# Kernel optimization log

Measured on AMD Instinct MI355X. Metric: run time of the kernel, lower is better.

The kernel has to match this reference:

```python
import jax, jax.numpy as jnp
import numpy as np

N_NODES = 100000
EPS = 1e-12  # F.normalize eps


def mean_aggregate(x, src, dst):
    # gather source features along edges, segment-mean into destinations
    msg = x[src]                                              # [E, D]
    summed = jax.ops.segment_sum(msg, dst, num_segments=N_NODES)  # [N, D]
    cnt = jax.ops.segment_sum(jnp.ones_like(dst, dtype=x.dtype), dst,
                              num_segments=N_NODES)           # [N]
    return summed / jnp.maximum(cnt, 1.0)[:, None]


def sage_conv(x, src, dst, W_l, b_l, W_r, normalize):
    agg = mean_aggregate(x, src, dst)
    out = agg @ W_l.T + b_l + x @ W_r.T  # lin_l(mean neigh) + lin_r(root)
    if normalize:
        norm = jnp.sqrt(jnp.sum(out * out, axis=-1, keepdims=True))
        out = out / jnp.maximum(norm, EPS)
    return out


def setup_inputs() -> dict:
    key = jax.random.key(0)
    ks = jax.random.split(key, 8)
    H, O = 128, 128
    s = 1.0 / np.sqrt(H)
    x = jax.random.normal(ks[0], (N_NODES, H), dtype=jnp.float32)
    edge_index = jax.random.randint(ks[1], (2, 1600000), 0, N_NODES, dtype=jnp.int64)
    return {
        "x": x,
        "edge_index": edge_index,
        "W1l": jax.random.uniform(ks[2], (H, H), jnp.float32, -s, s),
        "b1": jax.random.uniform(ks[3], (H,), jnp.float32, -s, s),
        "W1r": jax.random.uniform(ks[4], (H, H), jnp.float32, -s, s),
        "W2l": jax.random.uniform(ks[5], (O, H), jnp.float32, -s, s),
        "b2": jax.random.uniform(ks[6], (O,), jnp.float32, -s, s),
        "W2r": jax.random.uniform(ks[7], (O, H), jnp.float32, -s, s),
    }


def reference(x, edge_index, W1l, b1, W1r, W2l, b2, W2r):
    src, dst = edge_index[0], edge_index[1]
    h = sage_conv(x, src, dst, W1l, b1, W1r, normalize=True)
    h = jax.nn.relu(h)
    out = sage_conv(h, src, dst, W2l, b2, W2r, normalize=False)
    return out
```

## Files before the change

kernel.cpp:

```cpp
#include <hip/hip_runtime.h>
#include <hip/hip_bf16.h>
#include <hip/hip_fp16.h>

#define N_NODES 100000
#define DFEAT 128
#define SLAB 4096
#define BSHIFT 9
#define NBUCK 196

#define WS_CNT      0
#define WS_W16      100000
#define WS_BCNT     180000
#define WS_BBASE    180200
#define WS_BCUR     180400
#define WS_OFFS     200000
#define WS_ESRC     300608
#define WS_AGGH     1900608
#define WS_CASTH    8300608

typedef _Float16 half8 __attribute__((ext_vector_type(8)));
typedef _Float16 half2v __attribute__((ext_vector_type(2)));
typedef float floatx4 __attribute__((ext_vector_type(4)));

__global__ __launch_bounds__(256) void prep_kernel(const float* __restrict__ x,
                                                   __half* __restrict__ xh, int total4,
                                                   const int* __restrict__ dst,
                                                   int* __restrict__ bcnt,
                                                   const float* __restrict__ W1l,
                                                   const float* __restrict__ W1r,
                                                   const float* __restrict__ W2l,
                                                   const float* __restrict__ W2r,
                                                   __half* __restrict__ w16,
                                                   int E, int bpart, int castblocks) {
    __shared__ int lh[NBUCK];
    int b = blockIdx.x;
    if (b < castblocks) {
        int i = b * 256 + threadIdx.x;
        if (i < total4) {
            float4 v = ((const float4*)x)[i];
            __half2 h01 = __floats2half2_rn(v.x, v.y);
            __half2 h23 = __floats2half2_rn(v.z, v.w);
            uint2 o;
            o.x = *(unsigned int*)&h01;
            o.y = *(unsigned int*)&h23;
            ((uint2*)xh)[i] = o;
        }
        return;
    }
    if (b < castblocks + 64) {
        int i = (b - castblocks) * 256 + threadIdx.x;
        int m = i >> 12;
        int off = i & 4095;
        const float* Wp = (m == 0) ? W1l : (m == 1) ? W1r : (m == 2) ? W2l : W2r;
        float4 v = ((const float4*)Wp)[off];
        __half2 h01 = __floats2half2_rn(v.x, v.y);
        __half2 h23 = __floats2half2_rn(v.z, v.w);
        uint2 o;
        o.x = *(unsigned int*)&h01;
        o.y = *(unsigned int*)&h23;
        ((uint2*)w16)[i] = o;
        return;
    }
    int bb = b - castblocks - 64;
    for (int i = threadIdx.x; i < NBUCK; i += 256) lh[i] = 0;
    __syncthreads();
    int s0 = bb * SLAB, s1 = min(E, s0 + SLAB);
    for (int i = s0 + threadIdx.x; i < s1; i += 256)
        atomicAdd(&lh[dst[i] >> BSHIFT], 1);
    __syncthreads();
    for (int i = threadIdx.x; i < NBUCK; i += 256)
        if (lh[i] > 0) atomicAdd(&bcnt[i], lh[i]);
}

__global__ void bscan_kernel(const int* __restrict__ bcnt, int* __restrict__ bbase,
                             int* __restrict__ bcur, int E) {
    __shared__ int s[256];
    int t = threadIdx.x;
    int v = (t < NBUCK) ? bcnt[t] : 0;
    s[t] = v;
    __syncthreads();
    for (int d = 1; d < 256; d <<= 1) {
        int u = (t >= d) ? s[t - d] : 0;
        __syncthreads();
        s[t] += u;
        __syncthreads();
    }
    if (t < NBUCK) {
        int excl = s[t] - v;
        bbase[t] = excl;
        bcur[t] = excl;
    }
    if (t == 0) bbase[NBUCK] = E;
}

__global__ __launch_bounds__(256) void phase2_kernel(const int* __restrict__ src,
                                                     const int* __restrict__ dst,
                                                     int* __restrict__ bcur,
                                                     int2* __restrict__ pairs,
                                                     int E) {
    __shared__ int lbase[NBUCK];
    __shared__ int lcur[NBUCK];
    __shared__ int lgb[NBUCK];
    __shared__ int sc[256];
    __shared__ int2 lp[SLAB];
    int b = blockIdx.x;
    int t = threadIdx.x;
    for (int i = t; i < NBUCK; i += 256) lbase[i] = 0;
    __syncthreads();
    int s0 = b * SLAB, s1 = min(E, s0 + SLAB);
    for (int i = s0 + t; i < s1; i += 256)
        atomicAdd(&lbase[dst[i] >> BSHIFT], 1);
    __syncthreads();
    int v = (t < NBUCK) ? lbase[t] : 0;
    sc[t] = v;
    __syncthreads();
    for (int d = 1; d < 256; d <<= 1) {
        int u = (t >= d) ? sc[t - d] : 0;
        __syncthreads();
        sc[t] += u;
        __syncthreads();
    }
    if (t < NBUCK) {
        int excl = sc[t] - v;
        lbase[t] = excl;
        lcur[t] = excl;
        lgb[t] = (v > 0) ? atomicAdd(&bcur[t], v) : 0;
    }
    __syncthreads();
    for (int i = s0 + t; i < s1; i += 256) {
        int d = dst[i];
        int s = src[i];
        int bk = d >> BSHIFT;
        int pos = atomicAdd(&lcur[bk], 1);
        lp[pos] = make_int2(s, d);
    }
    __syncthreads();
    int m = s1 - s0;
    for (int i = t; i < m; i += 256) {
        int2 p = lp[i];
        int bk = p.y >> BSHIFT;
        pairs[lgb[bk] + (i - lbase[bk])] = p;
    }
}

__global__ __launch_bounds__(512) void phase3_kernel(const int2* __restrict__ pairs,
                                                     const int* __restrict__ bbase,
                                                     int* __restrict__ cnt,
                                                     int* __restrict__ offs,
                                                     int* __restrict__ esrc,
                                                     int n) {
    __shared__ int lcnt[512];
    __shared__ int sc[512];
    __shared__ int lexcl[512];
    int g = blockIdx.x;
    int node0 = g << BSHIFT;
    int t = threadIdx.x;
    lcnt[t] = 0;
    __syncthreads();
    int S = bbase[g];
    int Eg = bbase[g + 1];
    for (int i = S + t; i < Eg; i += 512)
        atomicAdd(&lcnt[pairs[i].y - node0], 1);
    __syncthreads();
    int v = lcnt[t];
    sc[t] = v;
    __syncthreads();
    for (int d = 1; d < 512; d <<= 1) {
        int u = (t >= d) ? sc[t - d] : 0;
        __syncthreads();
        sc[t] += u;
        __syncthreads();
    }
    int excl = sc[t] - v;
    lexcl[t] = excl;
    int nd = node0 + t;
    if (nd < n) {
        cnt[nd] = v;
        offs[nd] = S + excl;
    }
    __syncthreads();
    for (int i = S + t; i < Eg; i += 512) {
        int2 p = pairs[i];
        int pos = atomicAdd(&lexcl[p.y - node0], 1);
        esrc[S + pos] = p.x;
    }
}

#define ACC(c, r)                        \
    s[c][0] += *(half2v*)&(r).x;         \
    s[c][1] += *(half2v*)&(r).y;         \
    s[c][2] += *(half2v*)&(r).z;         \
    s[c][3] += *(half2v*)&(r).w;

__global__ void aggregate_kernel(const __half* __restrict__ feat, const int* __restrict__ esrc,
                                 const int* __restrict__ offs, const int* __restrict__ cnt,
                                 __half* __restrict__ agg, int n) {
    int wid = (blockIdx.x * blockDim.x + threadIdx.x) >> 6;
    int lane = threadIdx.x & 63;
    int grp = lane >> 4;
    int l15 = lane & 15;
    int node = wid * 4 + grp;
    if (node >= n) return;
    int beg = offs[node];
    int deg = cnt[node];
    const _Float16* fbase = (const _Float16*)feat + l15 * 8;
    const int* ep = esrc + beg;

    half2v s[4][4];
#pragma unroll
    for (int c = 0; c < 4; c++)
#pragma unroll
        for (int k = 0; k < 4; k++) s[c][k] = (half2v)(_Float16)0;

    int j = 0;
    for (; j + 8 <= deg; j += 8) {
        int i0 = ep[j + 0], i1 = ep[j + 1], i2 = ep[j + 2], i3 = ep[j + 3];
        int i4 = ep[j + 4], i5 = ep[j + 5], i6 = ep[j + 6], i7 = ep[j + 7];
        uint4 r0 = *(const uint4*)(fbase + (size_t)i0 * DFEAT);
        uint4 r1 = *(const uint4*)(fbase + (size_t)i1 * DFEAT);
        uint4 r2 = *(const uint4*)(fbase + (size_t)i2 * DFEAT);
        uint4 r3 = *(const uint4*)(fbase + (size_t)i3 * DFEAT);
        uint4 r4 = *(const uint4*)(fbase + (size_t)i4 * DFEAT);
        uint4 r5 = *(const uint4*)(fbase + (size_t)i5 * DFEAT);
        uint4 r6 = *(const uint4*)(fbase + (size_t)i6 * DFEAT);
        uint4 r7 = *(const uint4*)(fbase + (size_t)i7 * DFEAT);
        ACC(0, r0) ACC(1, r1) ACC(2, r2) ACC(3, r3)
        ACC(0, r4) ACC(1, r5) ACC(2, r6) ACC(3, r7)
    }
    for (; j + 4 <= deg; j += 4) {
        int i0 = ep[j + 0], i1 = ep[j + 1], i2 = ep[j + 2], i3 = ep[j + 3];
        uint4 r0 = *(const uint4*)(fbase + (size_t)i0 * DFEAT);
        uint4 r1 = *(const uint4*)(fbase + (size_t)i1 * DFEAT);
        uint4 r2 = *(const uint4*)(fbase + (size_t)i2 * DFEAT);
        uint4 r3 = *(const uint4*)(fbase + (size_t)i3 * DFEAT);
        ACC(0, r0) ACC(1, r1) ACC(2, r2) ACC(3, r3)
    }
    if (j < deg) {
        int rem = deg - j;
        int i0 = ep[j];
        int i1 = ep[j + (rem > 1 ? 1 : 0)];
        int i2 = ep[j + (rem > 2 ? 2 : 0)];
        uint4 r0 = *(const uint4*)(fbase + (size_t)i0 * DFEAT);
        uint4 r1 = *(const uint4*)(fbase + (size_t)i1 * DFEAT);
        uint4 r2 = *(const uint4*)(fbase + (size_t)i2 * DFEAT);
        if (rem < 2) { r1.x = 0u; r1.y = 0u; r1.z = 0u; r1.w = 0u; }
        if (rem < 3) { r2.x = 0u; r2.y = 0u; r2.z = 0u; r2.w = 0u; }
        ACC(0, r0) ACC(1, r1) ACC(2, r2)
    }

    float scale = 1.0f / fmaxf((float)deg, 1.0f);
    float a[8];
#pragma unroll
    for (int k = 0; k < 4; k++) {
        a[2 * k]     = ((float)s[0][k].x + (float)s[1][k].x) + ((float)s[2][k].x + (float)s[3][k].x);
        a[2 * k + 1] = ((float)s[0][k].y + (float)s[1][k].y) + ((float)s[2][k].y + (float)s[3][k].y);
    }
    __half2 h0 = __floats2half2_rn(a[0] * scale, a[1] * scale);
    __half2 h1 = __floats2half2_rn(a[2] * scale, a[3] * scale);
    __half2 h2 = __floats2half2_rn(a[4] * scale, a[5] * scale);
    __half2 h3 = __floats2half2_rn(a[6] * scale, a[7] * scale);
    uint4 o;
    o.x = *(unsigned int*)&h0;
    o.y = *(unsigned int*)&h1;
    o.z = *(unsigned int*)&h2;
    o.w = *(unsigned int*)&h3;
    *(uint4*)(agg + (size_t)node * DFEAT + l15 * 8) = o;
}

template <bool NORM_RELU>
__global__ __launch_bounds__(256) void gemm64_kernel(
    const __half* __restrict__ A1_, const __half* __restrict__ A2_,
    const __half* __restrict__ Wl16, const __half* __restrict__ Wr16,
    const float* __restrict__ bias, float* __restrict__ out32,
    __half* __restrict__ out16, int n) {
    __shared__ __align__(16) _Float16 lw[128 * 136];

    const _Float16* A1 = (const _Float16*)A1_;
    const _Float16* A2 = (const _Float16*)A2_;
    const _Float16* wl = (const _Float16*)Wl16;
    const _Float16* wr = (const _Float16*)Wr16;

    const int lane = threadIdx.x & 63;
    const int w = threadIdx.x >> 6;
    const int quad = lane >> 4;
    const int l15 = lane & 15;
    const int i0 = blockIdx.x * 64 + w * 16;
    int r = i0 + l15;
    if (r >= n) r = n - 1;
    const int kq = quad * 8;

    half8 bf[4];
#pragma unroll
    for (int k = 0; k < 4; k++)
        bf[k] = *(const half8*)(A1 + (size_t)r * DFEAT + k * 32 + kq);

    {
        int t = threadIdx.x;
        int row = t >> 1;
        int cb = (t & 1) * 64;
        const uint4* sp = (const uint4*)(wl + row * DFEAT + cb);
        uint4* dp = (uint4*)&lw[row * 136 + cb];
#pragma unroll
        for (int q = 0; q < 8; q++) dp[q] = sp[q];
    }
    __syncthreads();

    floatx4 acc[8];
#pragma unroll
    for (int ft = 0; ft < 8; ft++) acc[ft] = (floatx4){0.f, 0.f, 0.f, 0.f};

#pragma unroll
    for (int kci = 0; kci < 4; kci++) {
#pragma unroll
        for (int ft = 0; ft < 8; ft++) {
            half8 a = *(const half8*)&lw[(ft * 16 + l15) * 136 + kci * 32 + kq];
            acc[ft] = __builtin_amdgcn_mfma_f32_16x16x32_f16(a, bf[kci], acc[ft], 0, 0, 0);
        }
    }

    half8 xf[4];
#pragma unroll
    for (int k = 0; k < 4; k++)
        xf[k] = *(const half8*)(A2 + (size_t)r * DFEAT + k * 32 + kq);

    __syncthreads();
    {
        int t = threadIdx.x;
        int row = t >> 1;
        int cb = (t & 1) * 64;
        const uint4* sp = (const uint4*)(wr + row * DFEAT + cb);
        uint4* dp = (uint4*)&lw[row * 136 + cb];
#pragma unroll
        for (int q = 0; q < 8; q++) dp[q] = sp[q];
    }
    __syncthreads();

#pragma unroll
    for (int kci = 0; kci < 4; kci++) {
#pragma unroll
        for (int ft = 0; ft < 8; ft++) {
            half8 a = *(const half8*)&lw[(ft * 16 + l15) * 136 + kci * 32 + kq];
            acc[ft] = __builtin_amdgcn_mfma_f32_16x16x32_f16(a, xf[kci], acc[ft], 0, 0, 0);
        }
    }

    int node = i0 + l15;
    float v[8][4];
#pragma unroll
    for (int ft = 0; ft < 8; ft++) {
        const float4 bq = *(const float4*)(bias + ft * 16 + quad * 4);
        v[ft][0] = acc[ft][0] + bq.x;
        v[ft][1] = acc[ft][1] + bq.y;
        v[ft][2] = acc[ft][2] + bq.z;
        v[ft][3] = acc[ft][3] + bq.w;
    }
    if (NORM_RELU) {
        float ss = 0.f;
#pragma unroll
        for (int ft = 0; ft < 8; ft++)
#pragma unroll
            for (int q = 0; q < 4; q++) ss = fmaf(v[ft][q], v[ft][q], ss);
        ss += __shfl_xor(ss, 16);
        ss += __shfl_xor(ss, 32);
        float inv = 1.0f / fmaxf(sqrtf(ss), 1e-12f);
#pragma unroll
        for (int ft = 0; ft < 8; ft++)
#pragma unroll
            for (int q = 0; q < 4; q++) v[ft][q] = fmaxf(v[ft][q] * inv, 0.0f);
    }
    if (node < n) {
        if (NORM_RELU) {
            __half* op = (__half*)out16 + (size_t)node * DFEAT + quad * 4;
#pragma unroll
            for (int ft = 0; ft < 8; ft++) {
                __half2 h01 = __floats2half2_rn(v[ft][0], v[ft][1]);
                __half2 h23 = __floats2half2_rn(v[ft][2], v[ft][3]);
                uint2 o;
                o.x = *(unsigned int*)&h01;
                o.y = *(unsigned int*)&h23;
                *(uint2*)(op + ft * 16) = o;
            }
        } else {
            float* op = out32 + (size_t)node * DFEAT + quad * 4;
#pragma unroll
            for (int ft = 0; ft < 8; ft++)
                *(float4*)(op + ft * 16) = make_float4(v[ft][0], v[ft][1], v[ft][2], v[ft][3]);
        }
    }
}

extern "C" void kernel_launch(void* const* d_in, const int* in_sizes, int n_in,
                              void* d_out, int out_size, void* d_ws, size_t ws_size,
                              hipStream_t stream) {
    const float* x = (const float*)d_in[0];
    const int* edge_index = (const int*)d_in[1];
    const float* W1l = (const float*)d_in[2];
    const float* b1 = (const float*)d_in[3];
    const float* W1r = (const float*)d_in[4];
    const float* W2l = (const float*)d_in[5];
    const float* b2 = (const float*)d_in[6];
    const float* W2r = (const float*)d_in[7];
    float* out = (float*)d_out;

    const int E = in_sizes[1] / 2;
    const int n = in_sizes[0] / DFEAT;

    int* ws = (int*)d_ws;
    int* cnt = ws + WS_CNT;
    __half* w16 = (__half*)(ws + WS_W16);
    int* bcnt = ws + WS_BCNT;
    int* bbase = ws + WS_BBASE;
    int* bcur = ws + WS_BCUR;
    int* offs = ws + WS_OFFS;
    int* esrc = ws + WS_ESRC;
    int2* pairs = (int2*)(ws + WS_AGGH);
    __half* aggh = (__half*)(ws + WS_AGGH);
    __half* casth = (__half*)(ws + WS_CASTH);

    const int* src = edge_index;
    const int* dst = edge_index + E;

    const int bpart = (E + SLAB - 1) / SLAB;
    const int total4 = n * DFEAT / 4;
    const int castblocks = (total4 + 255) / 256;

    __half* w1l16 = w16;
    __half* w1r16 = w16 + 16384;
    __half* w2l16 = w16 + 32768;
    __half* w2r16 = w16 + 49152;

    hipMemsetAsync(bcnt, 0, NBUCK * sizeof(int), stream);

    prep_kernel<<<castblocks + 64 + bpart, 256, 0, stream>>>(
        x, casth, total4, dst, bcnt, W1l, W1r, W2l, W2r, w16, E, bpart, castblocks);
    bscan_kernel<<<1, 256, 0, stream>>>(bcnt, bbase, bcur, E);
    phase2_kernel<<<bpart, 256, 0, stream>>>(src, dst, bcur, pairs, E);
    phase3_kernel<<<NBUCK, 512, 0, stream>>>(pairs, bbase, cnt, offs, esrc, n);

    const int nwaves = (n + 3) / 4;
    const int aggb = (nwaves * 64 + 255) / 256;
    const int gemmb = (n + 63) / 64;

    aggregate_kernel<<<aggb, 256, 0, stream>>>(casth, esrc, offs, cnt, aggh, n);
    gemm64_kernel<true><<<gemmb, 256, 0, stream>>>(aggh, casth, w1l16, w1r16, b1,
                                                   nullptr, aggh, n);

    aggregate_kernel<<<aggb, 256, 0, stream>>>(aggh, esrc, offs, cnt, casth, n);
    gemm64_kernel<false><<<gemmb, 256, 0, stream>>>(casth, aggh, w2l16, w2r16, b2,
                                                    out, nullptr, n);
}
```

Measured before the change: 341.1 us.

## Fuse preprocessing and CSR build into one cooperative kernel with grid syncs

Replaces the memset plus four preprocessing launches (cast, bucket count, scan, bucket scatter, per-bucket sort) with a single cooperative persistent kernel that separates the phases with grid.sync. The aim is to remove launch overhead and inter-kernel gaps. In exchange, the grid is capped by occupancy (at most 1024 blocks), so the phases run as grid-stride loops with less parallelism. Phase 3 now runs with 256 threads per bucket instead of 512, and grid syncs have their own cost.

```diff
diff --git a/kernel.cpp b/kernel.cpp
--- a/kernel.cpp
+++ b/kernel.cpp
@@ -1,6 +1,9 @@
 #include <hip/hip_runtime.h>
 #include <hip/hip_bf16.h>
 #include <hip/hip_fp16.h>
+#include <hip/hip_cooperative_groups.h>
+
+namespace cg = cooperative_groups;
 
 #define N_NODES 100000
 #define DFEAT 128
@@ -22,35 +25,33 @@
 typedef _Float16 half2v __attribute__((ext_vector_type(2)));
 typedef float floatx4 __attribute__((ext_vector_type(4)));
 
-__global__ __launch_bounds__(256) void prep_kernel(const float* __restrict__ x,
-                                                   __half* __restrict__ xh, int total4,
-                                                   const int* __restrict__ dst,
-                                                   int* __restrict__ bcnt,
-                                                   const float* __restrict__ W1l,
-                                                   const float* __restrict__ W1r,
-                                                   const float* __restrict__ W2l,
-                                                   const float* __restrict__ W2r,
-                                                   __half* __restrict__ w16,
-                                                   int E, int bpart, int castblocks) {
-    __shared__ int lh[NBUCK];
-    int b = blockIdx.x;
-    if (b < castblocks) {
-        int i = b * 256 + threadIdx.x;
-        if (i < total4) {
-            float4 v = ((const float4*)x)[i];
-            __half2 h01 = __floats2half2_rn(v.x, v.y);
-            __half2 h23 = __floats2half2_rn(v.z, v.w);
-            uint2 o;
-            o.x = *(unsigned int*)&h01;
-            o.y = *(unsigned int*)&h23;
-            ((uint2*)xh)[i] = o;
-        }
-        return;
-    }
-    if (b < castblocks + 64) {
-        int i = (b - castblocks) * 256 + threadIdx.x;
-        int m = i >> 12;
-        int off = i & 4095;
+__global__ __launch_bounds__(256) void preprocess_coop(
+    const float* __restrict__ x, __half* __restrict__ xh, int total4,
+    const int* __restrict__ src, const int* __restrict__ dst,
+    int* __restrict__ bcnt, int* __restrict__ bbase, int* __restrict__ bcur,
+    const float* __restrict__ W1l, const float* __restrict__ W1r,
+    const float* __restrict__ W2l, const float* __restrict__ W2r,
+    __half* __restrict__ w16,
+    int2* __restrict__ pairs, int* __restrict__ cnt, int* __restrict__ offs,
+    int* __restrict__ esrc, int E, int bpart, int n)
+{
+    cg::grid_group grid = cg::this_grid();
+    __shared__ union {
+        int lh[NBUCK];
+        int bs[256];
+        struct { int lbase[NBUCK]; int lcur[NBUCK]; int lgb[NBUCK];
+                 int sc[256]; int2 lp[SLAB]; } d;
+        struct { int lcnt[512]; int sc[512]; int lexcl[512]; } e;
+    } sm;
+
+    const int t = threadIdx.x;
+    const int gtid = blockIdx.x * 256 + t;
+    const int gsz = gridDim.x * 256;
+
+    if (gtid < NBUCK) bcnt[gtid] = 0;
+    if (gtid < 16384) {
+        int m = gtid >> 12;
+        int off = gtid & 4095;
         const float* Wp = (m == 0) ? W1l : (m == 1) ? W1r : (m == 2) ? W2l : W2r;
         float4 v = ((const float4*)Wp)[off];
         __half2 h01 = __floats2half2_rn(v.x, v.y);
@@ -58,131 +59,131 @@
         uint2 o;
         o.x = *(unsigned int*)&h01;
         o.y = *(unsigned int*)&h23;
-        ((uint2*)w16)[i] = o;
-        return;
-    }
-    int bb = b - castblocks - 64;
-    for (int i = threadIdx.x; i < NBUCK; i += 256) lh[i] = 0;
-    __syncthreads();
-    int s0 = bb * SLAB, s1 = min(E, s0 + SLAB);
-    for (int i = s0 + threadIdx.x; i < s1; i += 256)
-        atomicAdd(&lh[dst[i] >> BSHIFT], 1);
-    __syncthreads();
-    for (int i = threadIdx.x; i < NBUCK; i += 256)
-        if (lh[i] > 0) atomicAdd(&bcnt[i], lh[i]);
-}
-
-__global__ void bscan_kernel(const int* __restrict__ bcnt, int* __restrict__ bbase,
-                             int* __restrict__ bcur, int E) {
-    __shared__ int s[256];
-    int t = threadIdx.x;
-    int v = (t < NBUCK) ? bcnt[t] : 0;
-    s[t] = v;
-    __syncthreads();
-    for (int d = 1; d < 256; d <<= 1) {
-        int u = (t >= d) ? s[t - d] : 0;
-        __syncthreads();
-        s[t] += u;
-        __syncthreads();
-    }
-    if (t < NBUCK) {
-        int excl = s[t] - v;
-        bbase[t] = excl;
-        bcur[t] = excl;
-    }
-    if (t == 0) bbase[NBUCK] = E;
-}
-
-__global__ __launch_bounds__(256) void phase2_kernel(const int* __restrict__ src,
-                                                     const int* __restrict__ dst,
-                                                     int* __restrict__ bcur,
-                                                     int2* __restrict__ pairs,
-                                                     int E) {
-    __shared__ int lbase[NBUCK];
-    __shared__ int lcur[NBUCK];
-    __shared__ int lgb[NBUCK];
-    __shared__ int sc[256];
-    __shared__ int2 lp[SLAB];
-    int b = blockIdx.x;
-    int t = threadIdx.x;
-    for (int i = t; i < NBUCK; i += 256) lbase[i] = 0;
-    __syncthreads();
-    int s0 = b * SLAB, s1 = min(E, s0 + SLAB);
-    for (int i = s0 + t; i < s1; i += 256)
-        atomicAdd(&lbase[dst[i] >> BSHIFT], 1);
-    __syncthreads();
-    int v = (t < NBUCK) ? lbase[t] : 0;
-    sc[t] = v;
-    __syncthreads();
-    for (int d = 1; d < 256; d <<= 1) {
-        int u = (t >= d) ? sc[t - d] : 0;
-        __syncthreads();
-        sc[t] += u;
-        __syncthreads();
-    }
-    if (t < NBUCK) {
-        int excl = sc[t] - v;
-        lbase[t] = excl;
-        lcur[t] = excl;
-        lgb[t] = (v > 0) ? atomicAdd(&bcur[t], v) : 0;
-    }
-    __syncthreads();
-    for (int i = s0 + t; i < s1; i += 256) {
-        int d = dst[i];
-        int s = src[i];
-        int bk = d >> BSHIFT;
-        int pos = atomicAdd(&lcur[bk], 1);
-        lp[pos] = make_int2(s, d);
-    }
-    __syncthreads();
-    int m = s1 - s0;
-    for (int i = t; i < m; i += 256) {
-        int2 p = lp[i];
-        int bk = p.y >> BSHIFT;
-        pairs[lgb[bk] + (i - lbase[bk])] = p;
-    }
-}
-
-__global__ __launch_bounds__(512) void phase3_kernel(const int2* __restrict__ pairs,
-                                                     const int* __restrict__ bbase,
-                                                     int* __restrict__ cnt,
-                                                     int* __restrict__ offs,
-                                                     int* __restrict__ esrc,
-                                                     int n) {
-    __shared__ int lcnt[512];
-    __shared__ int sc[512];
-    __shared__ int lexcl[512];
-    int g = blockIdx.x;
-    int node0 = g << BSHIFT;
-    int t = threadIdx.x;
-    lcnt[t] = 0;
-    __syncthreads();
-    int S = bbase[g];
-    int Eg = bbase[g + 1];
-    for (int i = S + t; i < Eg; i += 512)
-        atomicAdd(&lcnt[pairs[i].y - node0], 1);
-    __syncthreads();
-    int v = lcnt[t];
-    sc[t] = v;
-    __syncthreads();
-    for (int d = 1; d < 512; d <<= 1) {
-        int u = (t >= d) ? sc[t - d] : 0;
-        __syncthreads();
-        sc[t] += u;
-        __syncthreads();
-    }
-    int excl = sc[t] - v;
-    lexcl[t] = excl;
-    int nd = node0 + t;
-    if (nd < n) {
-        cnt[nd] = v;
-        offs[nd] = S + excl;
-    }
-    __syncthreads();
-    for (int i = S + t; i < Eg; i += 512) {
-        int2 p = pairs[i];
-        int pos = atomicAdd(&lexcl[p.y - node0], 1);
-        esrc[S + pos] = p.x;
+        ((uint2*)w16)[gtid] = o;
+    }
+    for (int i = gtid; i < total4; i += gsz) {
+        float4 v = ((const float4*)x)[i];
+        __half2 h01 = __floats2half2_rn(v.x, v.y);
+        __half2 h23 = __floats2half2_rn(v.z, v.w);
+        uint2 o;
+        o.x = *(unsigned int*)&h01;
+        o.y = *(unsigned int*)&h23;
+        ((uint2*)xh)[i] = o;
+    }
+    __threadfence();
+    grid.sync();
+
+    for (int sb = blockIdx.x; sb < bpart; sb += gridDim.x) {
+        for (int i = t; i < NBUCK; i += 256) sm.lh[i] = 0;
+        __syncthreads();
+        int s0 = sb * SLAB, s1 = min(E, s0 + SLAB);
+        for (int i = s0 + t; i < s1; i += 256)
+            atomicAdd(&sm.lh[dst[i] >> BSHIFT], 1);
+        __syncthreads();
+        for (int i = t; i < NBUCK; i += 256)
+            if (sm.lh[i] > 0) atomicAdd(&bcnt[i], sm.lh[i]);
+        __syncthreads();
+    }
+    __threadfence();
+    grid.sync();
+
+    if (blockIdx.x == 0) {
+        int v = (t < NBUCK) ? bcnt[t] : 0;
+        sm.bs[t] = v;
+        __syncthreads();
+        for (int d = 1; d < 256; d <<= 1) {
+            int u = (t >= d) ? sm.bs[t - d] : 0;
+            __syncthreads();
+            sm.bs[t] += u;
+            __syncthreads();
+        }
+        if (t < NBUCK) {
+            int excl = sm.bs[t] - v;
+            bbase[t] = excl;
+            bcur[t] = excl;
+        }
+        if (t == 0) bbase[NBUCK] = E;
+        __threadfence();
+    }
+    grid.sync();
+
+    for (int sb = blockIdx.x; sb < bpart; sb += gridDim.x) {
+        for (int i = t; i < NBUCK; i += 256) sm.d.lbase[i] = 0;
+        __syncthreads();
+        int s0 = sb * SLAB, s1 = min(E, s0 + SLAB);
+        for (int i = s0 + t; i < s1; i += 256)
+            atomicAdd(&sm.d.lbase[dst[i] >> BSHIFT], 1);
+        __syncthreads();
+        int v = (t < NBUCK) ? sm.d.lbase[t] : 0;
+        sm.d.sc[t] = v;
+        __syncthreads();
+        for (int d = 1; d < 256; d <<= 1) {
+            int u = (t >= d) ? sm.d.sc[t - d] : 0;
+            __syncthreads();
+            sm.d.sc[t] += u;
+            __syncthreads();
+        }
+        if (t < NBUCK) {
+            int excl = sm.d.sc[t] - v;
+            sm.d.lbase[t] = excl;
+            sm.d.lcur[t] = excl;
+            sm.d.lgb[t] = (v > 0) ? atomicAdd(&bcur[t], v) : 0;
+        }
+        __syncthreads();
+        for (int i = s0 + t; i < s1; i += 256) {
+            int dd = dst[i];
+            int ss = src[i];
+            int bk = dd >> BSHIFT;
+            int pos = atomicAdd(&sm.d.lcur[bk], 1);
+            sm.d.lp[pos] = make_int2(ss, dd);
+        }
+        __syncthreads();
+        int m = s1 - s0;
+        for (int i = t; i < m; i += 256) {
+            int2 p = sm.d.lp[i];
+            int bk = p.y >> BSHIFT;
+            pairs[sm.d.lgb[bk] + (i - sm.d.lbase[bk])] = p;
+        }
+        __syncthreads();
+    }
+    __threadfence();
+    grid.sync();
+
+    for (int g = blockIdx.x; g < NBUCK; g += gridDim.x) {
+        int node0 = g << BSHIFT;
+        sm.e.lcnt[t] = 0;
+        sm.e.lcnt[t + 256] = 0;
+        __syncthreads();
+        int S = bbase[g], Eg = bbase[g + 1];
+        for (int i = S + t; i < Eg; i += 256)
+            atomicAdd(&sm.e.lcnt[pairs[i].y - node0], 1);
+        __syncthreads();
+        int v0 = sm.e.lcnt[t], v1 = sm.e.lcnt[t + 256];
+        sm.e.sc[t] = v0;
+        sm.e.sc[t + 256] = v1;
+        __syncthreads();
+        for (int d = 1; d < 512; d <<= 1) {
+            int u0 = (t >= d) ? sm.e.sc[t - d] : 0;
+            int u1 = (t + 256 >= d) ? sm.e.sc[t + 256 - d] : 0;
+            __syncthreads();
+            sm.e.sc[t] += u0;
+            sm.e.sc[t + 256] += u1;
+            __syncthreads();
+        }
+        int e0 = sm.e.sc[t] - v0;
+        int e1 = sm.e.sc[t + 256] - v1;
+        sm.e.lexcl[t] = e0;
+        sm.e.lexcl[t + 256] = e1;
+        int nd0 = node0 + t, nd1 = node0 + t + 256;
+        if (nd0 < n) { cnt[nd0] = v0; offs[nd0] = S + e0; }
+        if (nd1 < n) { cnt[nd1] = v1; offs[nd1] = S + e1; }
+        __syncthreads();
+        for (int i = S + t; i < Eg; i += 256) {
+            int2 p = pairs[i];
+            int pos = atomicAdd(&sm.e.lexcl[p.y - node0], 1);
+            esrc[S + pos] = p.x;
+        }
+        __syncthreads();
     }
 }
 
@@ -402,8 +403,8 @@
     const float* W2r = (const float*)d_in[7];
     float* out = (float*)d_out;
 
-    const int E = in_sizes[1] / 2;
-    const int n = in_sizes[0] / DFEAT;
+    int E = in_sizes[1] / 2;
+    int n = in_sizes[0] / DFEAT;
 
     int* ws = (int*)d_ws;
     int* cnt = ws + WS_CNT;
@@ -420,22 +421,38 @@
     const int* src = edge_index;
     const int* dst = edge_index + E;
 
-    const int bpart = (E + SLAB - 1) / SLAB;
-    const int total4 = n * DFEAT / 4;
-    const int castblocks = (total4 + 255) / 256;
+    int bpart = (E + SLAB - 1) / SLAB;
+    int total4 = n * DFEAT / 4;
 
     __half* w1l16 = w16;
     __half* w1r16 = w16 + 16384;
     __half* w2l16 = w16 + 32768;
     __half* w2r16 = w16 + 49152;
 
-    hipMemsetAsync(bcnt, 0, NBUCK * sizeof(int), stream);
-
-    prep_kernel<<<castblocks + 64 + bpart, 256, 0, stream>>>(
-        x, casth, total4, dst, bcnt, W1l, W1r, W2l, W2r, w16, E, bpart, castblocks);
-    bscan_kernel<<<1, 256, 0, stream>>>(bcnt, bbase, bcur, E);
-    phase2_kernel<<<bpart, 256, 0, stream>>>(src, dst, bcur, pairs, E);
-    phase3_kernel<<<NBUCK, 512, 0, stream>>>(pairs, bbase, cnt, offs, esrc, n);
+    static int coopGrid = 0;
+    if (coopGrid == 0) {
+        int mb = 0;
+        if (hipOccupancyMaxActiveBlocksPerMultiprocessor(
+                &mb, reinterpret_cast<const void*>(&preprocess_coop), 256, 0) != hipSuccess ||
+            mb < 1)
+            mb = 2;
+        int ncu = 0;
+        if (hipDeviceGetAttribute(&ncu, hipDeviceAttributeMultiprocessorCount, 0) != hipSuccess ||
+            ncu <= 0)
+            ncu = 256;
+        long g = (long)mb * ncu;
+        coopGrid = (int)(g > 1024 ? 1024 : g);
+        if (coopGrid < 256) coopGrid = 256;
+    }
+
+    void* cargs[] = {
+        (void*)&x, (void*)&casth, (void*)&total4, (void*)&src, (void*)&dst,
+        (void*)&bcnt, (void*)&bbase, (void*)&bcur,
+        (void*)&W1l, (void*)&W1r, (void*)&W2l, (void*)&W2r, (void*)&w16,
+        (void*)&pairs, (void*)&cnt, (void*)&offs, (void*)&esrc,
+        (void*)&E, (void*)&bpart, (void*)&n};
+    (void)hipLaunchCooperativeKernel(reinterpret_cast<const void*>(&preprocess_coop),
+                                     dim3(coopGrid), dim3(256), cargs, 0, stream);
 
     const int nwaves = (n + 3) / 4;
     const int aggb = (nwaves * 64 + 255) / 256;
```

Result: slower. 938.8 us (+175.2%).

## Replace bucketed two-pass CSR build with global atomic histogram, scan, and scatter

Applied to the files above, without the earlier changes.

Replaces the bucket-partition CSR construction (bucket histogram, bucket scan, shared-memory partition into pairs, then per-bucket local sort) with a direct per-node global atomic histogram, a single-block scan over all node counts, and an atomic scatter of source indices. This removes the intermediate int2 pairs buffer and one full pass over the edges. In exchange it relies on global atomics to random addresses and a serial single-block scan over 100k nodes. Neighbor order within a node becomes nondeterministic, so fp16 summation order can vary between runs. The aggregate kernel now derives each node's start from the post-scatter offsets minus its degree.

```diff
diff --git a/kernel.cpp b/kernel.cpp
--- a/kernel.cpp
+++ b/kernel.cpp
@@ -4,15 +4,9 @@
 
 #define N_NODES 100000
 #define DFEAT 128
-#define SLAB 4096
-#define BSHIFT 9
-#define NBUCK 196
 
 #define WS_CNT      0
 #define WS_W16      100000
-#define WS_BCNT     180000
-#define WS_BBASE    180200
-#define WS_BCUR     180400
 #define WS_OFFS     200000
 #define WS_ESRC     300608
 #define WS_AGGH     1900608
@@ -25,14 +19,13 @@
 __global__ __launch_bounds__(256) void prep_kernel(const float* __restrict__ x,
                                                    __half* __restrict__ xh, int total4,
                                                    const int* __restrict__ dst,
-                                                   int* __restrict__ bcnt,
+                                                   int* __restrict__ cnt,
                                                    const float* __restrict__ W1l,
                                                    const float* __restrict__ W1r,
                                                    const float* __restrict__ W2l,
                                                    const float* __restrict__ W2r,
                                                    __half* __restrict__ w16,
-                                                   int E, int bpart, int castblocks) {
-    __shared__ int lh[NBUCK];
+                                                   int E, int castblocks) {
     int b = blockIdx.x;
     if (b < castblocks) {
         int i = b * 256 + threadIdx.x;
@@ -61,128 +54,43 @@
         ((uint2*)w16)[i] = o;
         return;
     }
-    int bb = b - castblocks - 64;
-    for (int i = threadIdx.x; i < NBUCK; i += 256) lh[i] = 0;
+    int hb = b - castblocks - 64;
+    int s0 = hb * 1024, s1 = min(E, s0 + 1024);
+    for (int i = s0 + threadIdx.x; i < s1; i += 256)
+        atomicAdd(&cnt[dst[i]], 1);
+}
+
+__global__ __launch_bounds__(1024) void scan_kernel(const int* __restrict__ cnt,
+                                                    int* __restrict__ offs, int n) {
+    __shared__ int ps[1024];
+    int t = threadIdx.x;
+    int chunk = (n + 1023) / 1024;
+    int s0 = t * chunk, s1 = min(n, s0 + chunk);
+    int sum = 0;
+    for (int i = s0; i < s1; i++) sum += cnt[i];
+    ps[t] = sum;
     __syncthreads();
-    int s0 = bb * SLAB, s1 = min(E, s0 + SLAB);
-    for (int i = s0 + threadIdx.x; i < s1; i += 256)
-        atomicAdd(&lh[dst[i] >> BSHIFT], 1);
-    __syncthreads();
-    for (int i = threadIdx.x; i < NBUCK; i += 256)
-        if (lh[i] > 0) atomicAdd(&bcnt[i], lh[i]);
-}
-
-__global__ void bscan_kernel(const int* __restrict__ bcnt, int* __restrict__ bbase,
-                             int* __restrict__ bcur, int E) {
-    __shared__ int s[256];
-    int t = threadIdx.x;
-    int v = (t < NBUCK) ? bcnt[t] : 0;
-    s[t] = v;
-    __syncthreads();
-    for (int d = 1; d < 256; d <<= 1) {
-        int u = (t >= d) ? s[t - d] : 0;
+    for (int d = 1; d < 1024; d <<= 1) {
+        int u = (t >= d) ? ps[t - d] : 0;
         __syncthreads();
-        s[t] += u;
+        ps[t] += u;
         __syncthreads();
     }
-    if (t < NBUCK) {
-        int excl = s[t] - v;
-        bbase[t] = excl;
-        bcur[t] = excl;
-    }
-    if (t == 0) bbase[NBUCK] = E;
-}
-
-__global__ __launch_bounds__(256) void phase2_kernel(const int* __restrict__ src,
-                                                     const int* __restrict__ dst,
-                                                     int* __restrict__ bcur,
-                                                     int2* __restrict__ pairs,
-                                                     int E) {
-    __shared__ int lbase[NBUCK];
-    __shared__ int lcur[NBUCK];
-    __shared__ int lgb[NBUCK];
-    __shared__ int sc[256];
-    __shared__ int2 lp[SLAB];
-    int b = blockIdx.x;
-    int t = threadIdx.x;
-    for (int i = t; i < NBUCK; i += 256) lbase[i] = 0;
-    __syncthreads();
-    int s0 = b * SLAB, s1 = min(E, s0 + SLAB);
-    for (int i = s0 + t; i < s1; i += 256)
-        atomicAdd(&lbase[dst[i] >> BSHIFT], 1);
-    __syncthreads();
-    int v = (t < NBUCK) ? lbase[t] : 0;
-    sc[t] = v;
-    __syncthreads();
-    for (int d = 1; d < 256; d <<= 1) {
-        int u = (t >= d) ? sc[t - d] : 0;
-        __syncthreads();
-        sc[t] += u;
-        __syncthreads();
-    }
-    if (t < NBUCK) {
-        int excl = sc[t] - v;
-        lbase[t] = excl;
-        lcur[t] = excl;
-        lgb[t] = (v > 0) ? atomicAdd(&bcur[t], v) : 0;
-    }
-    __syncthreads();
-    for (int i = s0 + t; i < s1; i += 256) {
-        int d = dst[i];
-        int s = src[i];
-        int bk = d >> BSHIFT;
-        int pos = atomicAdd(&lcur[bk], 1);
-        lp[pos] = make_int2(s, d);
-    }
-    __syncthreads();
-    int m = s1 - s0;
-    for (int i = t; i < m; i += 256) {
-        int2 p = lp[i];
-        int bk = p.y >> BSHIFT;
-        pairs[lgb[bk] + (i - lbase[bk])] = p;
-    }
-}
-
-__global__ __launch_bounds__(512) void phase3_kernel(const int2* __restrict__ pairs,
-                                                     const int* __restrict__ bbase,
-                                                     int* __restrict__ cnt,
-                                                     int* __restrict__ offs,
-                                                     int* __restrict__ esrc,
-                                                     int n) {
-    __shared__ int lcnt[512];
-    __shared__ int sc[512];
-    __shared__ int lexcl[512];
-    int g = blockIdx.x;
-    int node0 = g << BSHIFT;
-    int t = threadIdx.x;
-    lcnt[t] = 0;
-    __syncthreads();
-    int S = bbase[g];
-    int Eg = bbase[g + 1];
-    for (int i = S + t; i < Eg; i += 512)
-        atomicAdd(&lcnt[pairs[i].y - node0], 1);
-    __syncthreads();
-    int v = lcnt[t];
-    sc[t] = v;
-    __syncthreads();
-    for (int d = 1; d < 512; d <<= 1) {
-        int u = (t >= d) ? sc[t - d] : 0;
-        __syncthreads();
-        sc[t] += u;
-        __syncthreads();
-    }
-    int excl = sc[t] - v;
-    lexcl[t] = excl;
-    int nd = node0 + t;
-    if (nd < n) {
-        cnt[nd] = v;
-        offs[nd] = S + excl;
-    }
-    __syncthreads();
-    for (int i = S + t; i < Eg; i += 512) {
-        int2 p = pairs[i];
-        int pos = atomicAdd(&lexcl[p.y - node0], 1);
-        esrc[S + pos] = p.x;
+    int run = ps[t] - sum;
+    for (int i = s0; i < s1; i++) {
+        offs[i] = run;
+        run += cnt[i];
+    }
+}
+
+__global__ __launch_bounds__(256) void scatter_kernel(const int* __restrict__ src,
+                                                      const int* __restrict__ dst,
+                                                      int* __restrict__ offs,
+                                                      int* __restrict__ esrc, int E) {
+    int i = blockIdx.x * 256 + threadIdx.x;
+    if (i < E) {
+        int pos = atomicAdd(&offs[dst[i]], 1);
+        esrc[pos] = src[i];
     }
 }
 
@@ -201,8 +109,8 @@
     int l15 = lane & 15;
     int node = wid * 4 + grp;
     if (node >= n) return;
-    int beg = offs[node];
     int deg = cnt[node];
+    int beg = offs[node] - deg;
     const _Float16* fbase = (const _Float16*)feat + l15 * 8;
     const int* ep = esrc + beg;
 
@@ -402,40 +310,35 @@
     const float* W2r = (const float*)d_in[7];
     float* out = (float*)d_out;
 
-    const int E = in_sizes[1] / 2;
-    const int n = in_sizes[0] / DFEAT;
+    int E = in_sizes[1] / 2;
+    int n = in_sizes[0] / DFEAT;
 
     int* ws = (int*)d_ws;
     int* cnt = ws + WS_CNT;
     __half* w16 = (__half*)(ws + WS_W16);
-    int* bcnt = ws + WS_BCNT;
-    int* bbase = ws + WS_BBASE;
-    int* bcur = ws + WS_BCUR;
     int* offs = ws + WS_OFFS;
     int* esrc = ws + WS_ESRC;
-    int2* pairs = (int2*)(ws + WS_AGGH);
     __half* aggh = (__half*)(ws + WS_AGGH);
     __half* casth = (__half*)(ws + WS_CASTH);
 
     const int* src = edge_index;
     const int* dst = edge_index + E;
 
-    const int bpart = (E + SLAB - 1) / SLAB;
-    const int total4 = n * DFEAT / 4;
-    const int castblocks = (total4 + 255) / 256;
+    int total4 = n * DFEAT / 4;
+    int castblocks = (total4 + 255) / 256;
+    int histblocks = (E + 1023) / 1024;
 
     __half* w1l16 = w16;
     __half* w1r16 = w16 + 16384;
     __half* w2l16 = w16 + 32768;
     __half* w2r16 = w16 + 49152;
 
-    hipMemsetAsync(bcnt, 0, NBUCK * sizeof(int), stream);
-
-    prep_kernel<<<castblocks + 64 + bpart, 256, 0, stream>>>(
-        x, casth, total4, dst, bcnt, W1l, W1r, W2l, W2r, w16, E, bpart, castblocks);
-    bscan_kernel<<<1, 256, 0, stream>>>(bcnt, bbase, bcur, E);
-    phase2_kernel<<<bpart, 256, 0, stream>>>(src, dst, bcur, pairs, E);
-    phase3_kernel<<<NBUCK, 512, 0, stream>>>(pairs, bbase, cnt, offs, esrc, n);
+    hipMemsetAsync(cnt, 0, n * sizeof(int), stream);
+
+    prep_kernel<<<castblocks + 64 + histblocks, 256, 0, stream>>>(
+        x, casth, total4, dst, cnt, W1l, W1r, W2l, W2r, w16, E, castblocks);
+    scan_kernel<<<1, 1024, 0, stream>>>(cnt, offs, n);
+    scatter_kernel<<<(E + 255) / 256, 256, 0, stream>>>(src, dst, offs, esrc, E);
 
     const int nwaves = (n + 3) / 4;
     const int aggb = (nwaves * 64 + 255) / 256;
```

Result: slower. 622.5 us (+82.5%).

## Pack edge pairs into one int and read GEMM weights directly from global

Applied to the files above, without the earlier changes.

The bucketed edge pairs are packed into a single 32-bit word holding the low 9 bits of dst and a 17-bit src, which halves the intermediate pair traffic between phase2 and phase3. The GEMM kernel drops its LDS staging of the two weight matrices and the block barriers, loading weight fragments straight from global memory (expected to hit cache) and interleaving the left and right MFMAs. The packing assumes node ids fit in 17 bits (true for 100000 nodes). Weight reads now go through the cache hierarchy for every wave instead of once per block.

```diff
diff --git a/kernel.cpp b/kernel.cpp
--- a/kernel.cpp
+++ b/kernel.cpp
@@ -96,7 +96,7 @@
 __global__ __launch_bounds__(256) void phase2_kernel(const int* __restrict__ src,
                                                      const int* __restrict__ dst,
                                                      int* __restrict__ bcur,
-                                                     int2* __restrict__ pairs,
+                                                     int* __restrict__ pairs,
                                                      int E) {
     __shared__ int lbase[NBUCK];
     __shared__ int lcur[NBUCK];
@@ -139,11 +139,11 @@
     for (int i = t; i < m; i += 256) {
         int2 p = lp[i];
         int bk = p.y >> BSHIFT;
-        pairs[lgb[bk] + (i - lbase[bk])] = p;
-    }
-}
-
-__global__ __launch_bounds__(512) void phase3_kernel(const int2* __restrict__ pairs,
+        pairs[lgb[bk] + (i - lbase[bk])] = ((p.y & 511) << 17) | p.x;
+    }
+}
+
+__global__ __launch_bounds__(512) void phase3_kernel(const int* __restrict__ pairs,
                                                      const int* __restrict__ bbase,
                                                      int* __restrict__ cnt,
                                                      int* __restrict__ offs,
@@ -160,7 +160,7 @@
     int S = bbase[g];
     int Eg = bbase[g + 1];
     for (int i = S + t; i < Eg; i += 512)
-        atomicAdd(&lcnt[pairs[i].y - node0], 1);
+        atomicAdd(&lcnt[pairs[i] >> 17], 1);
     __syncthreads();
     int v = lcnt[t];
     sc[t] = v;
@@ -180,9 +180,9 @@
     }
     __syncthreads();
     for (int i = S + t; i < Eg; i += 512) {
-        int2 p = pairs[i];
-        int pos = atomicAdd(&lexcl[p.y - node0], 1);
-        esrc[S + pos] = p.x;
+        int p = pairs[i];
+        int pos = atomicAdd(&lexcl[p >> 17], 1);
+        esrc[S + pos] = p & 0x1FFFF;
     }
 }
 
@@ -273,8 +273,6 @@
     const __half* __restrict__ Wl16, const __half* __restrict__ Wr16,
     const float* __restrict__ bias, float* __restrict__ out32,
     __half* __restrict__ out16, int n) {
-    __shared__ __align__(16) _Float16 lw[128 * 136];
-
     const _Float16* A1 = (const _Float16*)A1_;
     const _Float16* A2 = (const _Float16*)A2_;
     const _Float16* wl = (const _Float16*)Wl16;
@@ -289,58 +287,26 @@
     if (r >= n) r = n - 1;
     const int kq = quad * 8;
 
-    half8 bf[4];
-#pragma unroll
-    for (int k = 0; k < 4; k++)
+    half8 bf[4], xf[4];
+#pragma unroll
+    for (int k = 0; k < 4; k++) {
         bf[k] = *(const half8*)(A1 + (size_t)r * DFEAT + k * 32 + kq);
-
-    {
-        int t = threadIdx.x;
-        int row = t >> 1;
-        int cb = (t & 1) * 64;
-        const uint4* sp = (const uint4*)(wl + row * DFEAT + cb);
-        uint4* dp = (uint4*)&lw[row * 136 + cb];
-#pragma unroll
-        for (int q = 0; q < 8; q++) dp[q] = sp[q];
-    }
-    __syncthreads();
+        xf[k] = *(const half8*)(A2 + (size_t)r * DFEAT + k * 32 + kq);
+    }
 
     floatx4 acc[8];
 #pragma unroll
     for (int ft = 0; ft < 8; ft++) acc[ft] = (floatx4){0.f, 0.f, 0.f, 0.f};
 
+    const int wrow = l15 * DFEAT + kq;
 #pragma unroll
     for (int kci = 0; kci < 4; kci++) {
 #pragma unroll
         for (int ft = 0; ft < 8; ft++) {
-            half8 a = *(const half8*)&lw[(ft * 16 + l15) * 136 + kci * 32 + kq];
-            acc[ft] = __builtin_amdgcn_mfma_f32_16x16x32_f16(a, bf[kci], acc[ft], 0, 0, 0);
-        }
-    }
-
-    half8 xf[4];
-#pragma unroll
-    for (int k = 0; k < 4; k++)
-        xf[k] = *(const half8*)(A2 + (size_t)r * DFEAT + k * 32 + kq);
-
-    __syncthreads();
-    {
-        int t = threadIdx.x;
-        int row = t >> 1;
-        int cb = (t & 1) * 64;
-        const uint4* sp = (const uint4*)(wr + row * DFEAT + cb);
-        uint4* dp = (uint4*)&lw[row * 136 + cb];
-#pragma unroll
-        for (int q = 0; q < 8; q++) dp[q] = sp[q];
-    }
-    __syncthreads();
-
-#pragma unroll
-    for (int kci = 0; kci < 4; kci++) {
-#pragma unroll
-        for (int ft = 0; ft < 8; ft++) {
-            half8 a = *(const half8*)&lw[(ft * 16 + l15) * 136 + kci * 32 + kq];
-            acc[ft] = __builtin_amdgcn_mfma_f32_16x16x32_f16(a, xf[kci], acc[ft], 0, 0, 0);
+            half8 al = *(const half8*)(wl + ft * 16 * DFEAT + wrow + kci * 32);
+            half8 ar = *(const half8*)(wr + ft * 16 * DFEAT + wrow + kci * 32);
+            acc[ft] = __builtin_amdgcn_mfma_f32_16x16x32_f16(al, bf[kci], acc[ft], 0, 0, 0);
+            acc[ft] = __builtin_amdgcn_mfma_f32_16x16x32_f16(ar, xf[kci], acc[ft], 0, 0, 0);
         }
     }
 
@@ -413,7 +379,7 @@
     int* bcur = ws + WS_BCUR;
     int* offs = ws + WS_OFFS;
     int* esrc = ws + WS_ESRC;
-    int2* pairs = (int2*)(ws + WS_AGGH);
+    int* pairs = ws + WS_AGGH;
     __half* aggh = (__half*)(ws + WS_AGGH);
     __half* casth = (__half*)(ws + WS_CASTH);
 
```

Measured after the change: 404.8 us. 18.7% more time.
